# Optimization experiments

Hardware: AMD Instinct MI355X
Metric: run time of the kernel (lower is better)

## Reference

```python
import jax, jax.numpy as jnp
import numpy as np

WEIGHT_FACTOR = 0.8


def _pairwise_l2(f):
    # ||a-b|| via GEMM trick: ||a||^2 + ||b||^2 - 2 a.b, avoiding the [N,N,D] blowup.
    sqn = jnp.sum(f * f, axis=1)                      # [N]
    sq = sqn[:, None] + sqn[None, :] - 2.0 * (f @ f.T)  # [N,N]
    sq = jnp.maximum(sq, 0.0)
    pos = sq > 0
    # safe sqrt: subgradient 0 at zero distance (matches torch.norm at 0)
    return jnp.where(pos, jnp.sqrt(jnp.where(pos, sq, 1.0)), 0.0)


def _mse(a, b):
    d = a - b
    return jnp.mean(d * d)


def setup_inputs() -> dict:
    key = jax.random.key(0)
    ks = jax.random.split(key, 8)
    N, D, C = 4096, 256, 1000
    return {
        "pred": jax.random.normal(ks[0], (N, C), dtype=jnp.float32),
        "target": jax.random.normal(ks[1], (N, C), dtype=jnp.float32),
        "pred_f0": jax.random.normal(ks[2], (N, D), dtype=jnp.float32),
        "pred_f1": jax.random.normal(ks[3], (N, D), dtype=jnp.float32),
        "pred_f2": jax.random.normal(ks[4], (N, D), dtype=jnp.float32),
        "target_f0": jax.random.normal(ks[5], (N, D), dtype=jnp.float32),
        "target_f1": jax.random.normal(ks[6], (N, D), dtype=jnp.float32),
        "target_f2": jax.random.normal(ks[7], (N, D), dtype=jnp.float32),
    }


def reference(pred, target, pred_f0, pred_f1, pred_f2, target_f0, target_f1, target_f2):
    pred_feats = (pred_f0, pred_f1, pred_f2)
    target_feats = (target_f0, target_f1, target_f2)
    num_features = len(pred_feats)

    label_loss = _mse(pred, target)
    feature_loss = 0.0
    for pf, tf in zip(pred_feats, target_feats):
        feature_loss = feature_loss + _mse(_pairwise_l2(pf), _pairwise_l2(tf))
    return (1.0 - WEIGHT_FACTOR) * label_loss + WEIGHT_FACTOR * feature_loss / num_features
```

## Files before the change

### kernel.cpp

```cpp
#include <hip/hip_runtime.h>
#include <stdint.h>

#define NR 4096
#define DD 256
#define NC_TOT 4096000
#define TILES 32
#define NTRI 528
#define NBLK_GRAM 512

typedef float f32x4 __attribute__((ext_vector_type(4)));
typedef unsigned char u8;

#define WS_MSEP_OFF  256
#define WS_FEATP_OFF 16384
#define WS_SQN_OFF   32768
#define WS_FP8_OFF   131072

__global__ __launch_bounds__(256) void prep_mse_kernel(
    const float* __restrict__ m0, const float* __restrict__ m1,
    const float* __restrict__ m2, const float* __restrict__ m3,
    const float* __restrict__ m4, const float* __restrict__ m5,
    const float4* __restrict__ pred, const float4* __restrict__ target,
    u8* __restrict__ q8, float* __restrict__ sqn, float* __restrict__ msep,
    unsigned* __restrict__ cnt)
{
    __shared__ float sr[4];
    const int t = threadIdx.x, w = t >> 6, lane = t & 63;
    const int y = blockIdx.y;
    if (y == 0 && blockIdx.x == 0 && t == 0) *cnt = 0u;

    if (y < 6) {
        const float* mp = m0;
        if (y == 1) mp = m1;
        else if (y == 2) mp = m2;
        else if (y == 3) mp = m3;
        else if (y == 4) mp = m4;
        else if (y == 5) mp = m5;
        const int R = blockIdx.x * 4 + w;
        const int P = R >> 7, rr = R & 127;
        const float4* src = (const float4*)(mp + (size_t)R * DD);
        float4 v = src[lane];
        float ss = v.x * v.x + v.y * v.y + v.z * v.z + v.w * v.w;
        unsigned lo = __builtin_amdgcn_cvt_pk_fp8_f32(v.x, v.y, 0u, false);
        unsigned hi = __builtin_amdgcn_cvt_pk_fp8_f32(v.z, v.w, 0u, false);
        unsigned packed = (lo & 0xffffu) | (hi << 16);
        size_t idx = ((size_t)(y * 32 + P) << 15)
                     + (size_t)(lane >> 1) * 1024 + rr * 8 + (lane & 1) * 4;
        *(unsigned*)(q8 + idx) = packed;
        #pragma unroll
        for (int off = 32; off; off >>= 1) ss += __shfl_down(ss, off);
        if (lane == 0) sqn[(size_t)y * NR + R] = ss;
    } else {
        const int b2 = (y - 6) * 1024 + blockIdx.x;
        float s = 0.f;
        for (int i = b2 * 256 + t; i < NC_TOT / 4; i += 2048 * 256) {
            float4 x = pred[i], yv = target[i];
            float dx = x.x - yv.x, dy = x.y - yv.y;
            float dz = x.z - yv.z, dw = x.w - yv.w;
            s += dx * dx + dy * dy + dz * dz + dw * dw;
        }
        #pragma unroll
        for (int off = 32; off; off >>= 1) s += __shfl_down(s, off);
        if (lane == 0) sr[w] = s;
        __syncthreads();
        if (t == 0) msep[b2] = sr[0] + sr[1] + sr[2] + sr[3];
    }
}

#define COMPUTE_STAGE(BI, ACC)                                                 \
  do {                                                                         \
    const u8* tA_ = &buf[BI][0];                                               \
    const u8* tB_ = &buf[BI][16384];                                           \
    __builtin_amdgcn_s_setprio(1);                                             \
    _Pragma("unroll")                                                          \
    for (int kc = 0; kc < 4; kc++) {                                           \
      const int gg = kc * 4 + quad;                                            \
      long a_[4], b_[2];                                                       \
      _Pragma("unroll")                                                        \
      for (int mi = 0; mi < 4; mi++)                                           \
        a_[mi] = *(const long*)&tA_[gg * 1024 + (wm * 64 + mi * 16 + l16) * 8];\
      _Pragma("unroll")                                                        \
      for (int ni = 0; ni < 2; ni++)                                           \
        b_[ni] = *(const long*)&tB_[gg * 1024 + (wn * 32 + ni * 16 + l16) * 8];\
      _Pragma("unroll")                                                        \
      for (int mi = 0; mi < 4; mi++)                                           \
        _Pragma("unroll")                                                      \
        for (int ni = 0; ni < 2; ni++)                                         \
          ACC[mi][ni] = __builtin_amdgcn_mfma_f32_16x16x32_fp8_fp8(            \
              a_[mi], b_[ni], ACC[mi][ni], 0, 0, 0);                           \
    }                                                                          \
    __builtin_amdgcn_s_setprio(0);                                             \
  } while (0)

#define RESET_ACC()                                                            \
  do {                                                                         \
    _Pragma("unroll")                                                          \
    for (int a4 = 0; a4 < 4; a4++)                                             \
      _Pragma("unroll")                                                        \
      for (int b2 = 0; b2 < 2; b2++) {                                         \
        accp[a4][b2] = f32x4{0.f, 0.f, 0.f, 0.f};                              \
        acct[a4][b2] = f32x4{0.f, 0.f, 0.f, 0.f};                              \
      }                                                                        \
  } while (0)

__global__ __launch_bounds__(512, 4) void gram_loss_kernel(
    const u8* __restrict__ q8, const float* __restrict__ sqn,
    float* __restrict__ featp, const float* __restrict__ msep,
    unsigned* __restrict__ cnt, float* __restrict__ out)
{
    __shared__ u8 buf[2][32768];
    __shared__ float s_red[8];
    __shared__ int s_last;

    const int xcd = blockIdx.x & 7, slot = blockIdx.x >> 3;
    const int t = threadIdx.x;
    const int w = t >> 6, lane = t & 63;
    const int wm = w >> 2, wn = w & 3;
    const int quad = lane >> 4, l16 = lane & 15;
    const char* qb = (const char*)q8;

    auto tile_of = [&](int k, int& f, int& ti, int& tj) -> bool {
        int rs = (slot + k * 21 + xcd * 9) & 63;
        int idx = rs + (k << 6), lin;
        if (xcd < 6) {
            if (idx >= 196) return false;
            f = xcd >> 1; lin = (xcd & 1) + 2 * idx;
        } else {
            if (idx >= 204) return false;
            int rr = (xcd - 6) + 2 * idx;
            f = rr / 136; lin = 392 + rr - f * 136;
        }
        int a = 0, rem = lin;
        while (rem >= TILES - a) { rem -= TILES - a; a++; }
        ti = a; tj = a + rem;
        return true;
    };

    auto prefetch = [&](int b, int f, int ti, int tj, int tgt, int kk) {
        const int m = f + 3 * tgt;
        const size_t bA = ((size_t)(m * 32 + ti)) << 15;
        const size_t bB = ((size_t)(m * 32 + tj)) << 15;
        const char* g = qb + ((w < 4) ? bA : bB) + kk * 16384
                        + (w & 3) * 4096 + lane * 16;
        char* l = (char*)&buf[b][0] + ((w < 4) ? 0 : 16384) + (w & 3) * 4096;
        #pragma unroll
        for (int i = 0; i < 4; i++)
            __builtin_amdgcn_global_load_lds(
                (const __attribute__((address_space(1))) void*)(g + i * 1024),
                (__attribute__((address_space(3))) void*)(l + i * 1024), 16, 0, 0);
    };

    f32x4 accp[4][2], acct[4][2];
    RESET_ACC();

    float local = 0.f;

    int fc, tic, tjc;
    tile_of(0, fc, tic, tjc);
    prefetch(0, fc, tic, tjc, 0, 0);
    __syncthreads();

    int k = 0;
    while (true) {
        prefetch(1, fc, tic, tjc, 0, 1);
        COMPUTE_STAGE(0, accp);
        __syncthreads();

        prefetch(0, fc, tic, tjc, 1, 0);
        COMPUTE_STAGE(1, accp);
        __syncthreads();

        prefetch(1, fc, tic, tjc, 1, 1);
        COMPUTE_STAGE(0, acct);
        __syncthreads();

        int fn, tin, tjn;
        const bool more = tile_of(k + 1, fn, tin, tjn);
        if (more) prefetch(0, fn, tin, tjn, 0, 0);
        COMPUTE_STAGE(1, acct);

        {
            const float* sqp = sqn + (size_t)fc * NR;
            const float* sqt = sqn + (size_t)(3 + fc) * NR;
            const bool diag = (tic == tjc);
            float tl = 0.f;
            #pragma unroll
            for (int mi = 0; mi < 4; mi++) {
                const int i0 = wm * 64 + mi * 16 + quad * 4;
                const f32x4 sip = *(const f32x4*)(sqp + tic * 128 + i0);
                const f32x4 sit = *(const f32x4*)(sqt + tic * 128 + i0);
                #pragma unroll
                for (int ni = 0; ni < 2; ni++) {
                    const int j_loc = wn * 32 + ni * 16 + l16;
                    const float spj = sqp[tjc * 128 + j_loc];
                    const float stj = sqt[tjc * 128 + j_loc];
                    const f32x4 gp = accp[mi][ni], gt = acct[mi][ni];
                    #pragma unroll
                    for (int r = 0; r < 4; r++) {
                        float dp2 = fmaxf(fmaf(-2.f, gp[r], sip[r] + spj), 0.f);
                        float dt2 = fmaxf(fmaf(-2.f, gt[r], sit[r] + stj), 0.f);
                        if (diag && (i0 + r == j_loc)) { dp2 = 0.f; dt2 = 0.f; }
                        float sq = __builtin_amdgcn_sqrtf(dp2 * dt2);
                        tl += fmaf(-2.f, sq, dp2 + dt2);
                    }
                }
            }
            local += diag ? tl : 2.f * tl;
            RESET_ACC();
        }
        __syncthreads();
        if (!more) break;
        k++;
        fc = fn; tic = tin; tjc = tjn;
    }

    #pragma unroll
    for (int off = 32; off; off >>= 1) local += __shfl_down(local, off);
    if (lane == 0) s_red[w] = local;
    __syncthreads();
    if (t == 0) {
        float bs = 0.f;
        #pragma unroll
        for (int i = 0; i < 8; i++) bs += s_red[i];
        featp[blockIdx.x] = bs;
        __threadfence();
        unsigned old = atomicAdd(cnt, 1u);
        s_last = (old == NBLK_GRAM - 1) ? 1 : 0;
    }
    __syncthreads();

    if (s_last) {
        __threadfence();
        float s2 = 0.f, m2 = 0.f;
        for (int i = t; i < NBLK_GRAM; i += 512) s2 += featp[i];
        for (int i = t; i < 2048; i += 512) m2 += msep[i];
        #pragma unroll
        for (int off = 32; off; off >>= 1) {
            s2 += __shfl_down(s2, off);
            m2 += __shfl_down(m2, off);
        }
        __shared__ float fr[8], mr[8];
        if (lane == 0) { fr[w] = s2; mr[w] = m2; }
        __syncthreads();
        if (t == 0) {
            float fs = 0.f, ms = 0.f;
            #pragma unroll
            for (int i = 0; i < 8; i++) { fs += fr[i]; ms += mr[i]; }
            out[0] = 0.2f * (ms / (float)NC_TOT) +
                     (0.8f / 3.0f) * (fs / ((float)NR * (float)NR));
        }
    }
}

extern "C" void kernel_launch(void* const* d_in, const int* in_sizes, int n_in,
                              void* d_out, int out_size, void* d_ws, size_t ws_size,
                              hipStream_t stream) {
    unsigned* cnt  = (unsigned*)d_ws;
    float* msep    = (float*)((char*)d_ws + WS_MSEP_OFF);
    float* featp   = (float*)((char*)d_ws + WS_FEATP_OFF);
    float* sqn     = (float*)((char*)d_ws + WS_SQN_OFF);
    u8* q8         = (u8*)((char*)d_ws + WS_FP8_OFF);

    prep_mse_kernel<<<dim3(1024, 8), 256, 0, stream>>>(
        (const float*)d_in[2], (const float*)d_in[3], (const float*)d_in[4],
        (const float*)d_in[5], (const float*)d_in[6], (const float*)d_in[7],
        (const float4*)d_in[0], (const float4*)d_in[1], q8, sqn, msep, cnt);

    gram_loss_kernel<<<NBLK_GRAM, 512, 0, stream>>>(
        q8, sqn, featp, msep, cnt, (float*)d_out);
}
```

Baseline: 140.2 us.

## Move label MSE reduction from prep kernel into gram kernel prologue

```diff
diff --git a/kernel.cpp b/kernel.cpp
--- a/kernel.cpp
+++ b/kernel.cpp
@@ -20,51 +20,32 @@
     const float* __restrict__ m0, const float* __restrict__ m1,
     const float* __restrict__ m2, const float* __restrict__ m3,
     const float* __restrict__ m4, const float* __restrict__ m5,
-    const float4* __restrict__ pred, const float4* __restrict__ target,
-    u8* __restrict__ q8, float* __restrict__ sqn, float* __restrict__ msep,
-    unsigned* __restrict__ cnt)
+    u8* __restrict__ q8, float* __restrict__ sqn, unsigned* __restrict__ cnt)
 {
-    __shared__ float sr[4];
     const int t = threadIdx.x, w = t >> 6, lane = t & 63;
     const int y = blockIdx.y;
     if (y == 0 && blockIdx.x == 0 && t == 0) *cnt = 0u;
 
-    if (y < 6) {
-        const float* mp = m0;
-        if (y == 1) mp = m1;
-        else if (y == 2) mp = m2;
-        else if (y == 3) mp = m3;
-        else if (y == 4) mp = m4;
-        else if (y == 5) mp = m5;
-        const int R = blockIdx.x * 4 + w;
-        const int P = R >> 7, rr = R & 127;
-        const float4* src = (const float4*)(mp + (size_t)R * DD);
-        float4 v = src[lane];
-        float ss = v.x * v.x + v.y * v.y + v.z * v.z + v.w * v.w;
-        unsigned lo = __builtin_amdgcn_cvt_pk_fp8_f32(v.x, v.y, 0u, false);
-        unsigned hi = __builtin_amdgcn_cvt_pk_fp8_f32(v.z, v.w, 0u, false);
-        unsigned packed = (lo & 0xffffu) | (hi << 16);
-        size_t idx = ((size_t)(y * 32 + P) << 15)
-                     + (size_t)(lane >> 1) * 1024 + rr * 8 + (lane & 1) * 4;
-        *(unsigned*)(q8 + idx) = packed;
-        #pragma unroll
-        for (int off = 32; off; off >>= 1) ss += __shfl_down(ss, off);
-        if (lane == 0) sqn[(size_t)y * NR + R] = ss;
-    } else {
-        const int b2 = (y - 6) * 1024 + blockIdx.x;
-        float s = 0.f;
-        for (int i = b2 * 256 + t; i < NC_TOT / 4; i += 2048 * 256) {
-            float4 x = pred[i], yv = target[i];
-            float dx = x.x - yv.x, dy = x.y - yv.y;
-            float dz = x.z - yv.z, dw = x.w - yv.w;
-            s += dx * dx + dy * dy + dz * dz + dw * dw;
-        }
-        #pragma unroll
-        for (int off = 32; off; off >>= 1) s += __shfl_down(s, off);
-        if (lane == 0) sr[w] = s;
-        __syncthreads();
-        if (t == 0) msep[b2] = sr[0] + sr[1] + sr[2] + sr[3];
-    }
+    const float* mp = m0;
+    if (y == 1) mp = m1;
+    else if (y == 2) mp = m2;
+    else if (y == 3) mp = m3;
+    else if (y == 4) mp = m4;
+    else if (y == 5) mp = m5;
+    const int R = blockIdx.x * 4 + w;
+    const int P = R >> 7, rr = R & 127;
+    const float4* src = (const float4*)(mp + (size_t)R * DD);
+    float4 v = src[lane];
+    float ss = v.x * v.x + v.y * v.y + v.z * v.z + v.w * v.w;
+    unsigned lo = __builtin_amdgcn_cvt_pk_fp8_f32(v.x, v.y, 0u, false);
+    unsigned hi = __builtin_amdgcn_cvt_pk_fp8_f32(v.z, v.w, 0u, false);
+    unsigned packed = (lo & 0xffffu) | (hi << 16);
+    size_t idx = ((size_t)(y * 32 + P) << 15)
+                 + (size_t)(lane >> 1) * 1024 + rr * 8 + (lane & 1) * 4;
+    *(unsigned*)(q8 + idx) = packed;
+    #pragma unroll
+    for (int off = 32; off; off >>= 1) ss += __shfl_down(ss, off);
+    if (lane == 0) sqn[(size_t)y * NR + R] = ss;
 }
 
 #define COMPUTE_STAGE(BI, ACC)                                                 \
@@ -105,11 +86,12 @@
 
 __global__ __launch_bounds__(512, 4) void gram_loss_kernel(
     const u8* __restrict__ q8, const float* __restrict__ sqn,
-    float* __restrict__ featp, const float* __restrict__ msep,
+    const float4* __restrict__ pred, const float4* __restrict__ target,
+    float* __restrict__ featp, float* __restrict__ msep,
     unsigned* __restrict__ cnt, float* __restrict__ out)
 {
     __shared__ u8 buf[2][32768];
-    __shared__ float s_red[8];
+    __shared__ float s_red[8], s_mse[8];
     __shared__ int s_last;
 
     const int xcd = blockIdx.x & 7, slot = blockIdx.x >> 3;
@@ -118,6 +100,14 @@
     const int wm = w >> 2, wn = w & 3;
     const int quad = lane >> 4, l16 = lane & 15;
     const char* qb = (const char*)q8;
+
+    float mse = 0.f;
+    for (int i = blockIdx.x * 512 + t; i < NC_TOT / 4; i += NBLK_GRAM * 512) {
+        float4 x = pred[i], yv = target[i];
+        float dx = x.x - yv.x, dy = x.y - yv.y;
+        float dz = x.z - yv.z, dw = x.w - yv.w;
+        mse += dx * dx + dy * dy + dz * dz + dw * dw;
+    }
 
     auto tile_of = [&](int k, int& f, int& ti, int& tj) -> bool {
         int rs = (slot + k * 21 + xcd * 9) & 63;
@@ -215,14 +205,18 @@
     }
 
     #pragma unroll
-    for (int off = 32; off; off >>= 1) local += __shfl_down(local, off);
-    if (lane == 0) s_red[w] = local;
+    for (int off = 32; off; off >>= 1) {
+        local += __shfl_down(local, off);
+        mse   += __shfl_down(mse, off);
+    }
+    if (lane == 0) { s_red[w] = local; s_mse[w] = mse; }
     __syncthreads();
     if (t == 0) {
-        float bs = 0.f;
+        float bs = 0.f, ms = 0.f;
         #pragma unroll
-        for (int i = 0; i < 8; i++) bs += s_red[i];
+        for (int i = 0; i < 8; i++) { bs += s_red[i]; ms += s_mse[i]; }
         featp[blockIdx.x] = bs;
+        msep[blockIdx.x]  = ms;
         __threadfence();
         unsigned old = atomicAdd(cnt, 1u);
         s_last = (old == NBLK_GRAM - 1) ? 1 : 0;
@@ -232,8 +226,10 @@
     if (s_last) {
         __threadfence();
         float s2 = 0.f, m2 = 0.f;
-        for (int i = t; i < NBLK_GRAM; i += 512) s2 += featp[i];
-        for (int i = t; i < 2048; i += 512) m2 += msep[i];
+        for (int i = t; i < NBLK_GRAM; i += 512) {
+            s2 += featp[i];
+            m2 += msep[i];
+        }
         #pragma unroll
         for (int off = 32; off; off >>= 1) {
             s2 += __shfl_down(s2, off);
@@ -261,11 +257,12 @@
     float* sqn     = (float*)((char*)d_ws + WS_SQN_OFF);
     u8* q8         = (u8*)((char*)d_ws + WS_FP8_OFF);
 
-    prep_mse_kernel<<<dim3(1024, 8), 256, 0, stream>>>(
+    prep_mse_kernel<<<dim3(1024, 6), 256, 0, stream>>>(
         (const float*)d_in[2], (const float*)d_in[3], (const float*)d_in[4],
         (const float*)d_in[5], (const float*)d_in[6], (const float*)d_in[7],
-        (const float4*)d_in[0], (const float4*)d_in[1], q8, sqn, msep, cnt);
+        q8, sqn, cnt);
 
     gram_loss_kernel<<<NBLK_GRAM, 512, 0, stream>>>(
-        q8, sqn, featp, msep, cnt, (float*)d_out);
+        q8, sqn, (const float4*)d_in[0], (const float4*)d_in[1],
+        featp, msep, cnt, (float*)d_out);
 }
```

Result: no change. 139.3 us (median of 2 runs) (-0.7%).
